# Kernel tuning notes

Hardware: AMD Instinct MI355X
Metric: run time of the kernel (lower is better)

## Reference

```python
import jax, jax.numpy as jnp
import numpy as np

EMBED = 768
GH = 4        # heads per group
GD = 256      # group dim = GH * head_dim
NSTEPS = 3    # n_pde_steps
DT = 0.05
HJ_H = 0.05   # Heimburg-Jackson dispersion coefficient


def _sh(u, k):
    # shift field content along sequence axis (axis=1) by k with zero boundary
    if k == 0:
        return u
    z = jnp.zeros_like(u)
    if k > 0:
        return z.at[:, k:, :].set(u[:, :-k, :])
    return z.at[:, :k, :].set(u[:, -k:, :])


def _d1(u):
    return 0.5 * (_sh(u, -1) - _sh(u, 1))


def _d2(u):
    return _sh(u, -1) - 2.0 * u + _sh(u, 1)


def _d3(u):
    return 0.5 * (_sh(u, -2) - 2.0 * _sh(u, -1) + 2.0 * _sh(u, 1) - _sh(u, 2))


def _d4(u):
    return _sh(u, -2) - 4.0 * _sh(u, -1) + 6.0 * u - 4.0 * _sh(u, 1) + _sh(u, 2)


def _attn(x, qkv_w, qkv_b, ow, ob, nh):
    # standard causal multi-head attention on one head group
    B, T, D = x.shape
    hd = D // nh
    qkv = x @ qkv_w + qkv_b                      # (B,T,3D)
    q, k, v = jnp.split(qkv, 3, axis=-1)
    heads = lambda a: a.reshape(B, T, nh, hd).transpose(0, 2, 1, 3)
    q, k, v = heads(q), heads(k), heads(v)
    s = jnp.einsum('bhqd,bhkd->bhqk', q, k) * (1.0 / np.sqrt(hd))
    causal = jnp.tril(jnp.ones((T, T), dtype=bool))
    s = jnp.where(causal, s, jnp.asarray(-1e9, s.dtype))
    p = jax.nn.softmax(s, axis=-1)
    o = jnp.einsum('bhqk,bhkd->bhqd', p, v).transpose(0, 2, 1, 3).reshape(B, T, D)
    return o @ ow + ob


def _sine_gordon(u):
    # u_tt = u_xx - sin(u), semi-implicit Euler (leapfrog-like)
    w = jnp.zeros_like(u)
    for _ in range(NSTEPS):
        w = w + DT * (_d2(u) - jnp.sin(u))
        u = u + DT * w
    return u


def _kdv(u):
    # u_t = -6 u u_x - u_xxx, explicit Euler
    for _ in range(NSTEPS):
        u = u + DT * (-6.0 * u * _d1(u) - _d3(u))
    return u


def _hj(u):
    # Heimburg-Jackson: u_tt = d_xx((c0^2 + p u + q u^2) u) - h u_xxxx
    # with c0=1, p=-1, q=1
    w = jnp.zeros_like(u)
    for _ in range(NSTEPS):
        f = u - u * u + u * u * u
        w = w + DT * (_d2(f) - HJ_H * _d4(u))
        u = u + DT * w
    return u


def setup_inputs() -> dict:
    key = jax.random.key(0)
    ks = jax.random.split(key, 16)
    s = 0.02
    d, gd = EMBED, GD
    inp = {'x': jax.random.normal(ks[0], (4, 2048, d), dtype=jnp.float32)}
    inp['in_w'] = jax.random.normal(ks[1], (d, d), jnp.float32) * s
    inp['in_b'] = jnp.zeros((d,), jnp.float32)
    for i, n in enumerate(['sg', 'kdv', 'hj']):
        inp[n + '_qkv_w'] = jax.random.normal(ks[2 + 4 * i], (gd, 3 * gd), jnp.float32) * s
        inp[n + '_qkv_b'] = jnp.zeros((3 * gd,), jnp.float32)
        inp[n + '_out_w'] = jax.random.normal(ks[3 + 4 * i], (gd, gd), jnp.float32) * s
        inp[n + '_out_b'] = jnp.zeros((gd,), jnp.float32)
    inp['out_w'] = jax.random.normal(ks[14], (d, d), jnp.float32) * s
    inp['out_b'] = jnp.zeros((d,), jnp.float32)
    return inp


def reference(x, in_w, in_b,
              sg_qkv_w, sg_qkv_b, sg_out_w, sg_out_b,
              kdv_qkv_w, kdv_qkv_b, kdv_out_w, kdv_out_b,
              hj_qkv_w, hj_qkv_b, hj_out_w, hj_out_b,
              out_w, out_b):
    h = x @ in_w + in_b
    xg = jnp.split(h, [GD, 2 * GD], axis=-1)
    sg = _sine_gordon(_attn(xg[0], sg_qkv_w, sg_qkv_b, sg_out_w, sg_out_b, GH))
    kv = _kdv(_attn(xg[1], kdv_qkv_w, kdv_qkv_b, kdv_out_w, kdv_out_b, GH))
    hj = _hj(_attn(xg[2], hj_qkv_w, hj_qkv_b, hj_out_w, hj_out_b, GH))
    out = jnp.concatenate([sg, kv, hj], axis=-1)
    return out @ out_w + out_b
```

## Files before the change

kernel.cpp:

```cpp
#include <hip/hip_runtime.h>
#include <math.h>

#define B_   4
#define T_   2048
#define D_   768
#define M_   8192
#define GD_  256
#define NH_  4
#define HD_  64

typedef short  s16x8 __attribute__((ext_vector_type(8)));
typedef __bf16 bfx8  __attribute__((ext_vector_type(8)));
typedef float  fx4   __attribute__((ext_vector_type(4)));

#define LOG2E 1.44269504088896f
#define QSCALE (0.125f * LOG2E)

__device__ __forceinline__ short f2bf(float f) {
  union { float f; unsigned u; } v; v.f = f;
  unsigned r = v.u + 0x7fffu + ((v.u >> 16) & 1u);
  return (short)(r >> 16);
}

__device__ __forceinline__ unsigned cvt_pk_bf16(float lo, float hi) {
  unsigned r;
  asm("v_cvt_pk_bf16_f32 %0, %1, %2" : "=v"(r) : "v"(lo), "v"(hi));
  return r;
}

__device__ __forceinline__ void gload16(const void* g, void* l) {
  __builtin_amdgcn_global_load_lds(
      (const __attribute__((address_space(1))) unsigned int*)g,
      (__attribute__((address_space(3))) unsigned int*)l, 16, 0, 0);
}

struct PW { const short* p0; const short* p1; const short* p2; };
struct PB { const float* p0; const float* p1; const float* p2; };
__device__ __forceinline__ const short* selw(const PW& s, int z) {
  return z == 0 ? s.p0 : (z == 1 ? s.p1 : s.p2);
}
__device__ __forceinline__ const float* selb(const PB& s, int z) {
  return z == 0 ? s.p0 : (z == 1 ? s.p1 : s.p2);
}

template<int AT, int OBF, int MODE, int BM>
__global__ __launch_bounds__(256) void gemm_mfma(
    const void* __restrict__ Avoid, long sA, int lda,
    PW Wp, PB Bp, int K,
    void* __restrict__ C, long sC, int ldc,
    void* __restrict__ xtra)
{
  constexpr int NF = BM / 32;
  constexpr int WTM = BM / 2;
  __shared__ short As[2][BM * 64];
  __shared__ short Bs[AT ? 1 : 2][128 * 64];

  const int z = blockIdx.z;
  const short* Ab16 = (const short*)Avoid + (long)z * sA;
  const float* Ab32 = (const float*)Avoid + (long)z * sA;
  const short* Wb = selw(Wp, z);
  const float* bb = selb(Bp, z);

  const int nx = gridDim.x, nwg = nx * gridDim.y;
  const int orig = blockIdx.y * nx + blockIdx.x;
  const int xcd = orig & 7, loc = orig >> 3;
  const int qq = nwg >> 3, rr = nwg & 7;
  const int wg = (xcd < rr ? xcd * (qq + 1) : rr * (qq + 1) + (xcd - rr) * qq) + loc;
  const int n0 = (wg % nx) * 128;
  const int m0 = (wg / nx) * BM;

  const int tid = threadIdx.x, lane = tid & 63, w = tid >> 6;
  const int wm = w >> 1, wn = w & 1;
  const int quad = lane >> 4, mr = lane & 15;

  fx4 acc[NF][4] = {};

  auto compute = [&](const short* Ab, const short* Bb) {
#pragma unroll
    for (int ks = 0; ks < 2; ++ks) {
      const int cc = ks * 32 + quad * 8;
      const int swz = cc ^ ((mr & 7) * 8);
      bfx8 af[NF], bf[4];
#pragma unroll
      for (int i = 0; i < NF; ++i)
        af[i] = *(const bfx8*)&Ab[(wm * WTM + i * 16 + mr) * 64 + swz];
#pragma unroll
      for (int j = 0; j < 4; ++j)
        bf[j] = *(const bfx8*)&Bb[(wn * 64 + j * 16 + mr) * 64 + swz];
#pragma unroll
      for (int i = 0; i < NF; ++i)
#pragma unroll
        for (int j = 0; j < 4; ++j)
          acc[i][j] = __builtin_amdgcn_mfma_f32_16x16x32_bf16(af[i], bf[j], acc[i][j], 0, 0, 0);
    }
  };

  if (AT) {
    const int r0 = tid >> 3;
    const int cs = (tid & 7) * 8;
    const int wswz = cs ^ ((r0 & 7) * 8);
    s16x8 ar[NF], br[4];

    auto loadA = [&](int k0) {
#pragma unroll
      for (int gg = 0; gg < NF; ++gg) {
        const float* p = Ab32 + (long)(m0 + r0 + 32 * gg) * lda + k0 + cs;
        float4 f0 = *(const float4*)p;
        float4 f1 = *(const float4*)(p + 4);
        short o[8] = { f2bf(f0.x), f2bf(f0.y), f2bf(f0.z), f2bf(f0.w),
                       f2bf(f1.x), f2bf(f1.y), f2bf(f1.z), f2bf(f1.w) };
        ar[gg] = *(s16x8*)o;
      }
    };
    auto loadB = [&](int k0) {
#pragma unroll
      for (int hh = 0; hh < 4; ++hh)
        br[hh] = *(const s16x8*)(Wb + (long)(n0 + r0 + 32 * hh) * K + k0 + cs);
    };

    loadA(0); loadB(0);
    for (int k0 = 0; k0 < K; k0 += 64) {
      asm volatile("s_waitcnt vmcnt(0)" ::: "memory");
#pragma unroll
      for (int gg = 0; gg < NF; ++gg)
        *(s16x8*)&As[0][(r0 + 32 * gg) * 64 + wswz] = ar[gg];
#pragma unroll
      for (int hh = 0; hh < 4; ++hh)
        *(s16x8*)&Bs[0][(r0 + 32 * hh) * 64 + wswz] = br[hh];
      asm volatile("s_waitcnt lgkmcnt(0)" ::: "memory");
      __builtin_amdgcn_s_barrier();
      if (k0 + 64 < K) { loadA(k0 + 64); loadB(k0 + 64); }
      compute(&As[0][0], &Bs[0][0]);
      __builtin_amdgcn_s_barrier();
    }
  } else {
    const int lrow = lane >> 3, lcol = lane & 7;

    auto stageA = [&](short* dst, int k0) {
#pragma unroll
      for (int i = 0; i < NF; ++i) {
        const int r = i * 32 + w * 8 + lrow;
        const int swz = (lcol * 8) ^ ((r & 7) * 8);
        gload16(Ab16 + (long)(m0 + r) * lda + k0 + swz,
                dst + (i * 32 + w * 8) * 64);
      }
    };
    auto stageB = [&](short* dst, int k0) {
#pragma unroll
      for (int i = 0; i < 4; ++i) {
        const int r = i * 32 + w * 8 + lrow;
        const int swz = (lcol * 8) ^ ((r & 7) * 8);
        gload16(Wb + (long)(n0 + r) * K + k0 + swz,
                dst + (i * 32 + w * 8) * 64);
      }
    };

    stageA(&As[0][0], 0); stageB(&Bs[0][0], 0);
    const int NT = K >> 6;
    for (int t = 0; t < NT; ++t) {
      const int cur = t & 1;
      if (t + 1 < NT) {
        stageA(&As[cur ^ 1][0], (t + 1) * 64);
        stageB(&Bs[cur ^ 1][0], (t + 1) * 64);
        if constexpr (BM == 128)
          asm volatile("s_waitcnt vmcnt(8)" ::: "memory");
        else
          asm volatile("s_waitcnt vmcnt(6)" ::: "memory");
      } else {
        asm volatile("s_waitcnt vmcnt(0)" ::: "memory");
      }
      __builtin_amdgcn_s_barrier();
      compute(&As[cur][0], &Bs[cur][0]);
      __builtin_amdgcn_s_barrier();
    }
  }

  float* Cf = (float*)C + (long)z * sC;
  short* Cs = (short*)C + (long)z * sC;
#pragma unroll
  for (int j = 0; j < 4; ++j) {
    const int col = n0 + wn * 64 + j * 16 + mr;
    const float bvx = bb[col];
#pragma unroll
    for (int i = 0; i < NF; ++i) {
      const int row0 = m0 + wm * WTM + i * 16 + quad * 4;
      if (MODE == 2) {
        const int rb = row0 >> 11, t0 = row0 & 2047;
        fx4 o;
#pragma unroll
        for (int r = 0; r < 4; ++r) o[r] = acc[i][j][r] + bvx;
        *(fx4*)((float*)xtra + (((long)z * B_ + rb) * GD_ + col) * T_ + t0) = o;
      } else if (MODE == 1 && col >= 512) {
        const int h = (col - 512) >> 6, hd = (col - 512) & 63;
        const int rb = row0 >> 11, t0 = row0 & 2047;
        short o4[4];
#pragma unroll
        for (int r = 0; r < 4; ++r) o4[r] = f2bf(acc[i][j][r] + bvx);
        *(short4*)((short*)xtra + ((((long)z * B_ + rb) * NH_ + h) * HD_ + hd) * T_ + t0) =
            *(short4*)o4;
      } else {
        const float sc = (MODE == 1 && col < 256) ? QSCALE : 1.0f;
#pragma unroll
        for (int r = 0; r < 4; ++r) {
          float v = (acc[i][j][r] + bvx) * sc;
          if (OBF) Cs[(long)(row0 + r) * ldc + col] = f2bf(v);
          else     Cf[(long)(row0 + r) * ldc + col] = v;
        }
      }
    }
  }
}

__global__ __launch_bounds__(256) void cvt_kernel(
    const float* __restrict__ x, short* __restrict__ xb)
{
  const size_t i = ((size_t)blockIdx.x * 256 + threadIdx.x) * 8;
  float4 f0 = *(const float4*)(x + i);
  float4 f1 = *(const float4*)(x + i + 4);
  short o[8] = { f2bf(f0.x), f2bf(f0.y), f2bf(f0.z), f2bf(f0.w),
                 f2bf(f1.x), f2bf(f1.y), f2bf(f1.z), f2bf(f1.w) };
  *(s16x8*)(xb + i) = *(s16x8*)o;
}

__global__ __launch_bounds__(256) void flash_attn_mfma(
    short* __restrict__ qkv, const short* __restrict__ vtb)
{
  __shared__ short Ks[64][72];
  __shared__ short Vs[80][72];
  __shared__ short Ps[64 * 64];

  const int bid = blockIdx.x;
  const int Q = 31 - (bid / 48);
  const int combo = bid % 48;
  const int g = combo % 3, bh = combo / 3;
  const int b = bh >> 2, h = bh & 3;

  short* base = qkv + ((size_t)g * M_ + (size_t)b * T_) * D_;
  short*       Qp = base + h * HD_;
  const short* Kp = base + GD_ + h * HD_;
  const short* Vtp = vtb + ((((size_t)g * B_ + b) * NH_ + h) * HD_) * T_;

  const int tid = threadIdx.x, lane = tid & 63, w = tid >> 6;
  const int quad = lane >> 4, mr = lane & 15;
  const int q0 = Q * 64, wr = w * 16;

  const int sra = tid >> 3, sc = (tid & 7) * 8;

  if (tid < 128) {
    const short ov = 0x3F80;
    s16x8 one = { ov, ov, ov, ov, ov, ov, ov, ov };
    *(s16x8*)&Vs[64 + (tid >> 3)][(tid & 7) * 8] = one;
  }

  bfx8 aq[2];
#pragma unroll
  for (int ks = 0; ks < 2; ++ks)
    aq[ks] = *(const bfx8*)(Qp + (size_t)(q0 + wr + mr) * D_ +
                            ks * 32 + quad * 8);

  s16x8 kreg0 = *(const s16x8*)(Kp + (size_t)sra * D_ + sc);
  s16x8 kreg1 = *(const s16x8*)(Kp + (size_t)(sra + 32) * D_ + sc);
  s16x8 vreg0 = *(const s16x8*)(Vtp + (size_t)sra * T_ + sc);
  s16x8 vreg1 = *(const s16x8*)(Vtp + (size_t)(sra + 32) * T_ + sc);

  fx4 Oa[5] = {};

  char* PsB = (char*)&Ps[0];
  const int rot = (mr & 7) << 4;

  for (int kt = 0; kt <= Q; ++kt) {
    *(s16x8*)&Ks[sra][sc]      = kreg0;
    *(s16x8*)&Ks[sra + 32][sc] = kreg1;
    *(s16x8*)&Vs[sra][sc]      = vreg0;
    *(s16x8*)&Vs[sra + 32][sc] = vreg1;
    __syncthreads();

    if (kt < Q) {
      const int kn = (kt + 1) * 64;
      kreg0 = *(const s16x8*)(Kp + (size_t)(kn + sra) * D_ + sc);
      kreg1 = *(const s16x8*)(Kp + (size_t)(kn + sra + 32) * D_ + sc);
      vreg0 = *(const s16x8*)(Vtp + (size_t)sra * T_ + kn + sc);
      vreg1 = *(const s16x8*)(Vtp + (size_t)(sra + 32) * T_ + kn + sc);
    }

    fx4 st[4] = {};
#pragma unroll
    for (int ks = 0; ks < 2; ++ks) {
      bfx8 bk[4];
#pragma unroll
      for (int jj = 0; jj < 4; ++jj)
        bk[jj] = *(const bfx8*)&Ks[jj * 16 + mr][ks * 32 + quad * 8];
#pragma unroll
      for (int jj = 0; jj < 4; ++jj)
        st[jj] = __builtin_amdgcn_mfma_f32_16x16x32_bf16(bk[jj], aq[ks], st[jj], 0, 0, 0);
    }

    if (kt == Q) {
      const int qg = q0 + wr + mr;
#pragma unroll
      for (int jj = 0; jj < 4; ++jj) {
        const int kvg0 = kt * 64 + jj * 16 + quad * 4;
#pragma unroll
        for (int r = 0; r < 4; ++r)
          if (kvg0 + r > qg) st[jj][r] = -1e30f;
      }
    }

    {
      const int rowb = (wr + mr) << 7;
#pragma unroll
      for (int jj = 0; jj < 4; ++jj) {
        float e0 = exp2f(st[jj][0]);
        float e1 = exp2f(st[jj][1]);
        float e2 = exp2f(st[jj][2]);
        float e3 = exp2f(st[jj][3]);
        unsigned pk0 = cvt_pk_bf16(e0, e1);
        unsigned pk1 = cvt_pk_bf16(e2, e3);
        unsigned long long pv = (unsigned long long)pk0 |
                                ((unsigned long long)pk1 << 32);
        const int kb = (jj * 32 + quad * 8) ^ rot;
        *(unsigned long long*)(PsB + rowb + kb) = pv;
      }
    }

#pragma unroll
    for (int ks = 0; ks < 2; ++ks) {
      const int rowb = (wr + mr) << 7;
      const int kb = (ks * 64 + quad * 16) ^ rot;
      bfx8 ap = *(const bfx8*)(PsB + rowb + kb);
#pragma unroll
      for (int j = 0; j < 5; ++j) {
        bfx8 bv = *(const bfx8*)&Vs[j * 16 + mr][ks * 32 + quad * 8];
        Oa[j] = __builtin_amdgcn_mfma_f32_16x16x32_bf16(ap, bv, Oa[j], 0, 0, 0);
      }
    }
    __syncthreads();
  }

#pragma unroll
  for (int r = 0; r < 4; ++r) {
    const float inv = 1.0f / Oa[4][r];
    const int row = q0 + wr + quad * 4 + r;
#pragma unroll
    for (int j = 0; j < 4; ++j)
      Qp[(size_t)row * D_ + j * 16 + mr] = f2bf(Oa[j][r] * inv);
  }
}

__device__ __forceinline__ float fhj(float x) { return x - x * x + x * x * x; }

__global__ __launch_bounds__(256) void pde_kernel(
    const float* __restrict__ ut, short* __restrict__ ubt)
{
  __shared__ float halo[3][2][4];

  const int cg = blockIdx.x, b = blockIdx.y, g = blockIdx.z;
  const int tid = threadIdx.x, w = tid >> 6, lane = tid & 63;
  const int c = w >> 1, half = w & 1;
  const int t0 = half * 1024 + lane * 16;
  const float dt = 0.05f;

  const float* src = ut + (((size_t)g * B_ + b) * GD_ + cg * 2 + c) * T_ + t0;

  float uc[20];
#pragma unroll
  for (int q = 0; q < 4; ++q)
    *(fx4*)&uc[2 + q * 4] = *(const fx4*)(src + q * 4);

  {
    float h0 = __shfl_up(uc[16], 1);
    float h1 = __shfl_up(uc[17], 1);
    float h2 = __shfl_down(uc[2], 1);
    float h3 = __shfl_down(uc[3], 1);
    if (half == 0 && lane == 63) { halo[0][c][0] = uc[16]; halo[0][c][1] = uc[17]; }
    if (half == 1 && lane == 0)  { halo[0][c][2] = uc[2];  halo[0][c][3] = uc[3]; }
    __syncthreads();
    uc[0] = h0; uc[1] = h1; uc[18] = h2; uc[19] = h3;
    if (lane == 0) {
      if (half == 1) { uc[0] = halo[0][c][0]; uc[1] = halo[0][c][1]; }
      else           { uc[0] = 0.f;           uc[1] = 0.f; }
    }
    if (lane == 63) {
      if (half == 0) { uc[18] = halo[0][c][2]; uc[19] = halo[0][c][3]; }
      else           { uc[18] = 0.f;           uc[19] = 0.f; }
    }
  }

  float wreg[16];
#pragma unroll
  for (int i = 0; i < 16; ++i) wreg[i] = 0.f;

  for (int step = 0; step < 3; ++step) {
    float nu[16];
#pragma unroll
    for (int tt = 0; tt < 16; ++tt) {
      float um2 = uc[tt], um1 = uc[tt + 1], u = uc[tt + 2];
      float up1 = uc[tt + 3], up2 = uc[tt + 4];
      if (g == 0) {
        float d2 = up1 - 2.f * u + um1;
        wreg[tt] += dt * (d2 - __sinf(u));
        nu[tt] = u + dt * wreg[tt];
      } else if (g == 1) {
        float d1 = 0.5f * (up1 - um1);
        float d3 = 0.5f * (up2 - 2.f * up1 + 2.f * um1 - um2);
        nu[tt] = u + dt * (-6.f * u * d1 - d3);
      } else {
        float d2f = fhj(up1) - 2.f * fhj(u) + fhj(um1);
        float d4  = up2 - 4.f * up1 + 6.f * u - 4.f * um1 + um2;
        wreg[tt] += dt * (d2f - 0.05f * d4);
        nu[tt] = u + dt * wreg[tt];
      }
    }
    if (step < 2) {
      float h0 = __shfl_up(nu[14], 1);
      float h1 = __shfl_up(nu[15], 1);
      float h2 = __shfl_down(nu[0], 1);
      float h3 = __shfl_down(nu[1], 1);
      if (half == 0 && lane == 63) { halo[step + 1][c][0] = nu[14]; halo[step + 1][c][1] = nu[15]; }
      if (half == 1 && lane == 0)  { halo[step + 1][c][2] = nu[0];  halo[step + 1][c][3] = nu[1]; }
      __syncthreads();
      uc[0] = h0; uc[1] = h1; uc[18] = h2; uc[19] = h3;
      if (lane == 0) {
        if (half == 1) { uc[0] = halo[step + 1][c][0]; uc[1] = halo[step + 1][c][1]; }
        else           { uc[0] = 0.f;                  uc[1] = 0.f; }
      }
      if (lane == 63) {
        if (half == 0) { uc[18] = halo[step + 1][c][2]; uc[19] = halo[step + 1][c][3]; }
        else           { uc[18] = 0.f;                  uc[19] = 0.f; }
      }
    }
#pragma unroll
    for (int i = 0; i < 16; ++i) uc[2 + i] = nu[i];
  }

  short o16[16];
#pragma unroll
  for (int i = 0; i < 16; ++i) o16[i] = f2bf(uc[2 + i]);
  short* dst = ubt + (((size_t)g * B_ + b) * GD_ + cg * 2 + c) * T_ + t0;
#pragma unroll
  for (int q = 0; q < 2; ++q)
    *(s16x8*)(dst + q * 8) = *(s16x8*)&o16[q * 8];
}

__global__ __launch_bounds__(256) void transp_kernel(
    const short* __restrict__ ubt, short* __restrict__ ub)
{
  __shared__ short Ls[32][264];

  const int tt = blockIdx.x;
  const int ct = blockIdx.y;
  const int z  = blockIdx.z;
  const int g = z >> 2, b = z & 3;
  const int tid = threadIdx.x;
  const int c0 = ct * 32, t0 = tt * 256;

  const short* src = ubt + (((size_t)g * B_ + b) * GD_ + c0) * T_ + t0;
#pragma unroll
  for (int it = 0; it < 4; ++it) {
    const int row = (tid >> 5) + it * 8;
    const int col = (tid & 31) * 8;
    *(s16x8*)&Ls[row][col] = *(const s16x8*)(src + (size_t)row * T_ + col);
  }
  __syncthreads();

  short* dst = ub + (size_t)b * T_ * D_ + g * GD_ + c0;
  const int cq = tid & 7, tr = tid >> 3;
#pragma unroll
  for (int p = 0; p < 8; ++p) {
    const int tl = p * 32 + tr;
    short o4[4];
#pragma unroll
    for (int i = 0; i < 4; ++i) o4[i] = Ls[cq * 4 + i][tl];
    *(short4*)(dst + (size_t)(t0 + tl) * D_ + cq * 4) = *(short4*)o4;
  }
}

struct PrepArgs {
  const float* w[8]; short* wt[8];
  int K[8], N[8];
  int tend[8];
};

__global__ __launch_bounds__(256) void prep_kernel(PrepArgs pa)
{
  const int bid = blockIdx.x, tid = threadIdx.x;
  __shared__ float Ws[32][33];
  int ti = 0;
#pragma unroll
  for (int i = 0; i < 8; ++i) if (bid >= pa.tend[i]) ti = i + 1;
  const int tloc = bid - (ti ? pa.tend[ti - 1] : 0);
  const int K = pa.K[ti], N = pa.N[ti];
  const int ntx = N >> 5;
  const int k0 = (tloc / ntx) * 32, n0 = (tloc % ntx) * 32;
  const float* W = pa.w[ti];
  short* WT = pa.wt[ti];
  const int tx = tid & 31, ty = tid >> 5;

#pragma unroll
  for (int i = 0; i < 4; ++i)
    Ws[ty + 8 * i][tx] = W[(long)(k0 + ty + 8 * i) * N + n0 + tx];
  __syncthreads();
#pragma unroll
  for (int i = 0; i < 4; ++i) {
    int r = ty + 8 * i;
    WT[(long)(n0 + r) * K + k0 + tx] = f2bf(Ws[tx][r]);
  }
}

extern "C" void kernel_launch(void* const* d_in, const int* in_sizes, int n_in,
                              void* d_out, int out_size, void* d_ws, size_t ws_size,
                              hipStream_t stream)
{
  (void)in_sizes; (void)n_in; (void)out_size; (void)ws_size;

  const float* x         = (const float*)d_in[0];
  const float* in_w      = (const float*)d_in[1];
  const float* in_b      = (const float*)d_in[2];
  const float* sg_qkv_w  = (const float*)d_in[3];
  const float* sg_qkv_b  = (const float*)d_in[4];
  const float* sg_out_w  = (const float*)d_in[5];
  const float* sg_out_b  = (const float*)d_in[6];
  const float* kdv_qkv_w = (const float*)d_in[7];
  const float* kdv_qkv_b = (const float*)d_in[8];
  const float* kdv_out_w = (const float*)d_in[9];
  const float* kdv_out_b = (const float*)d_in[10];
  const float* hj_qkv_w  = (const float*)d_in[11];
  const float* hj_qkv_b  = (const float*)d_in[12];
  const float* hj_out_w  = (const float*)d_in[13];
  const float* hj_out_b  = (const float*)d_in[14];
  const float* out_w     = (const float*)d_in[15];
  const float* out_b     = (const float*)d_in[16];
  float* out = (float*)d_out;

  const size_t MD = (size_t)M_ * D_;
  short* base = (short*)d_ws;
  short* xb   = base;
  short* hb   = base + MD;
  float* uf   = (float*)d_ws;
  short* qkvb = base + 2 * MD;
  short* ub16 = qkvb + 3 * MD;
  short* wts  = ub16 + MD;
  short* in_wT  = wts;
  short* qkvT0  = in_wT + 589824;
  short* qkvT1  = qkvT0 + 196608;
  short* qkvT2  = qkvT1 + 196608;
  short* outT0  = qkvT2 + 196608;
  short* outT1  = outT0 + 65536;
  short* outT2  = outT1 + 65536;
  short* out_wT = outT2 + 65536;
  short* vtb    = out_wT + 589824;
  short* ubt    = qkvb;

  dim3 blk(256);

  PrepArgs pa;
  const float* wsrc[8] = { in_w, sg_qkv_w, kdv_qkv_w, hj_qkv_w,
                           sg_out_w, kdv_out_w, hj_out_w, out_w };
  short* wdst[8] = { in_wT, qkvT0, qkvT1, qkvT2, outT0, outT1, outT2, out_wT };
  int Ksz[8] = { 768, 256, 256, 256, 256, 256, 256, 768 };
  int Nsz[8] = { 768, 768, 768, 768, 256, 256, 256, 768 };
  int cum = 0;
  for (int i = 0; i < 8; ++i) {
    pa.w[i] = wsrc[i]; pa.wt[i] = wdst[i]; pa.K[i] = Ksz[i]; pa.N[i] = Nsz[i];
    cum += (Ksz[i] >> 5) * (Nsz[i] >> 5);
    pa.tend[i] = cum;
  }
  prep_kernel<<<dim3((unsigned)cum), blk, 0, stream>>>(pa);
  cvt_kernel<<<dim3((unsigned)(MD / 2048)), blk, 0, stream>>>(x, xb);

  gemm_mfma<0, 1, 0, 64><<<dim3(6, 128, 1), blk, 0, stream>>>(
      xb, 0, D_, PW{in_wT, in_wT, in_wT}, PB{in_b, in_b, in_b}, D_,
      hb, 0, D_, nullptr);

  gemm_mfma<0, 1, 1, 64><<<dim3(6, 128, 3), blk, 0, stream>>>(
      hb, 256, D_,
      PW{qkvT0, qkvT1, qkvT2}, PB{sg_qkv_b, kdv_qkv_b, hj_qkv_b}, GD_,
      qkvb, (long)MD, D_, vtb);

  flash_attn_mfma<<<dim3(1536), blk, 0, stream>>>(qkvb, vtb);

  gemm_mfma<0, 0, 2, 64><<<dim3(2, 128, 3), blk, 0, stream>>>(
      qkvb, (long)MD, D_,
      PW{outT0, outT1, outT2}, PB{sg_out_b, kdv_out_b, hj_out_b}, GD_,
      uf, 0, 0, uf);

  pde_kernel<<<dim3(128, 4, 3), blk, 0, stream>>>(uf, ubt);

  transp_kernel<<<dim3(8, 8, 12), blk, 0, stream>>>(ubt, ub16);

  gemm_mfma<0, 0, 0, 64><<<dim3(6, 128, 1), blk, 0, stream>>>(
      ub16, 0, D_, PW{out_wT, out_wT, out_wT}, PB{out_b, out_b, out_b}, D_,
      out, 0, D_, nullptr);
}
```

Baseline: 257.6 us.

## Double flash-attention query tile to 128 rows with 512-thread blocks

Each attention block now covers 128 query rows using 8 waves instead of 64 rows with 4 waves, so every K/V tile staged in shared memory is reused by twice as many waves. Each thread loads one K and one V vector per tile instead of two, and the grid is halved. Waves whose rows lie entirely before the current causal tile skip the compute but still join the barriers, which adds some idle time on the diagonal tiles and lowers the number of blocks available to fill the GPU.

```diff
diff --git a/kernel.cpp b/kernel.cpp
--- a/kernel.cpp
+++ b/kernel.cpp
@@ -222,15 +222,15 @@
   *(s16x8*)(xb + i) = *(s16x8*)o;
 }
 
-__global__ __launch_bounds__(256) void flash_attn_mfma(
+__global__ __launch_bounds__(512) void flash_attn_mfma(
     short* __restrict__ qkv, const short* __restrict__ vtb)
 {
   __shared__ short Ks[64][72];
   __shared__ short Vs[80][72];
-  __shared__ short Ps[64 * 64];
+  __shared__ short Ps[128 * 64];
 
   const int bid = blockIdx.x;
-  const int Q = 31 - (bid / 48);
+  const int Q = 15 - (bid / 48);
   const int combo = bid % 48;
   const int g = combo % 3, bh = combo / 3;
   const int b = bh >> 2, h = bh & 3;
@@ -242,7 +242,8 @@
 
   const int tid = threadIdx.x, lane = tid & 63, w = tid >> 6;
   const int quad = lane >> 4, mr = lane & 15;
-  const int q0 = Q * 64, wr = w * 16;
+  const int q0 = Q * 128, wr = w * 16;
+  const int qhi = q0 + wr + 15;
 
   const int sra = tid >> 3, sc = (tid & 7) * 8;
 
@@ -258,80 +259,77 @@
     aq[ks] = *(const bfx8*)(Qp + (size_t)(q0 + wr + mr) * D_ +
                             ks * 32 + quad * 8);
 
-  s16x8 kreg0 = *(const s16x8*)(Kp + (size_t)sra * D_ + sc);
-  s16x8 kreg1 = *(const s16x8*)(Kp + (size_t)(sra + 32) * D_ + sc);
-  s16x8 vreg0 = *(const s16x8*)(Vtp + (size_t)sra * T_ + sc);
-  s16x8 vreg1 = *(const s16x8*)(Vtp + (size_t)(sra + 32) * T_ + sc);
+  s16x8 kreg = *(const s16x8*)(Kp + (size_t)sra * D_ + sc);
+  s16x8 vreg = *(const s16x8*)(Vtp + (size_t)sra * T_ + sc);
 
   fx4 Oa[5] = {};
 
   char* PsB = (char*)&Ps[0];
   const int rot = (mr & 7) << 4;
 
-  for (int kt = 0; kt <= Q; ++kt) {
-    *(s16x8*)&Ks[sra][sc]      = kreg0;
-    *(s16x8*)&Ks[sra + 32][sc] = kreg1;
-    *(s16x8*)&Vs[sra][sc]      = vreg0;
-    *(s16x8*)&Vs[sra + 32][sc] = vreg1;
+  const int ktmax = 2 * Q + 1;
+  for (int kt = 0; kt <= ktmax; ++kt) {
+    *(s16x8*)&Ks[sra][sc] = kreg;
+    *(s16x8*)&Vs[sra][sc] = vreg;
     __syncthreads();
 
-    if (kt < Q) {
+    if (kt < ktmax) {
       const int kn = (kt + 1) * 64;
-      kreg0 = *(const s16x8*)(Kp + (size_t)(kn + sra) * D_ + sc);
-      kreg1 = *(const s16x8*)(Kp + (size_t)(kn + sra + 32) * D_ + sc);
-      vreg0 = *(const s16x8*)(Vtp + (size_t)sra * T_ + kn + sc);
-      vreg1 = *(const s16x8*)(Vtp + (size_t)(sra + 32) * T_ + kn + sc);
-    }
-
-    fx4 st[4] = {};
-#pragma unroll
-    for (int ks = 0; ks < 2; ++ks) {
-      bfx8 bk[4];
-#pragma unroll
-      for (int jj = 0; jj < 4; ++jj)
-        bk[jj] = *(const bfx8*)&Ks[jj * 16 + mr][ks * 32 + quad * 8];
-#pragma unroll
-      for (int jj = 0; jj < 4; ++jj)
-        st[jj] = __builtin_amdgcn_mfma_f32_16x16x32_bf16(bk[jj], aq[ks], st[jj], 0, 0, 0);
-    }
-
-    if (kt == Q) {
-      const int qg = q0 + wr + mr;
-#pragma unroll
-      for (int jj = 0; jj < 4; ++jj) {
-        const int kvg0 = kt * 64 + jj * 16 + quad * 4;
-#pragma unroll
-        for (int r = 0; r < 4; ++r)
-          if (kvg0 + r > qg) st[jj][r] = -1e30f;
-      }
-    }
-
-    {
-      const int rowb = (wr + mr) << 7;
-#pragma unroll
-      for (int jj = 0; jj < 4; ++jj) {
-        float e0 = exp2f(st[jj][0]);
-        float e1 = exp2f(st[jj][1]);
-        float e2 = exp2f(st[jj][2]);
-        float e3 = exp2f(st[jj][3]);
-        unsigned pk0 = cvt_pk_bf16(e0, e1);
-        unsigned pk1 = cvt_pk_bf16(e2, e3);
-        unsigned long long pv = (unsigned long long)pk0 |
-                                ((unsigned long long)pk1 << 32);
-        const int kb = (jj * 32 + quad * 8) ^ rot;
-        *(unsigned long long*)(PsB + rowb + kb) = pv;
-      }
-    }
-
-#pragma unroll
-    for (int ks = 0; ks < 2; ++ks) {
-      const int rowb = (wr + mr) << 7;
-      const int kb = (ks * 64 + quad * 16) ^ rot;
-      bfx8 ap = *(const bfx8*)(PsB + rowb + kb);
-#pragma unroll
-      for (int j = 0; j < 5; ++j) {
-        bfx8 bv = *(const bfx8*)&Vs[j * 16 + mr][ks * 32 + quad * 8];
-        Oa[j] = __builtin_amdgcn_mfma_f32_16x16x32_bf16(ap, bv, Oa[j], 0, 0, 0);
+      kreg = *(const s16x8*)(Kp + (size_t)(kn + sra) * D_ + sc);
+      vreg = *(const s16x8*)(Vtp + (size_t)sra * T_ + kn + sc);
+    }
+
+    if (kt * 64 <= qhi) {
+      fx4 st[4] = {};
+#pragma unroll
+      for (int ks = 0; ks < 2; ++ks) {
+        bfx8 bk[4];
+#pragma unroll
+        for (int jj = 0; jj < 4; ++jj)
+          bk[jj] = *(const bfx8*)&Ks[jj * 16 + mr][ks * 32 + quad * 8];
+#pragma unroll
+        for (int jj = 0; jj < 4; ++jj)
+          st[jj] = __builtin_amdgcn_mfma_f32_16x16x32_bf16(bk[jj], aq[ks], st[jj], 0, 0, 0);
+      }
+
+      if (kt >= 2 * Q) {
+        const int qg = q0 + wr + mr;
+#pragma unroll
+        for (int jj = 0; jj < 4; ++jj) {
+          const int kvg0 = kt * 64 + jj * 16 + quad * 4;
+#pragma unroll
+          for (int r = 0; r < 4; ++r)
+            if (kvg0 + r > qg) st[jj][r] = -1e30f;
+        }
+      }
+
+      {
+        const int rowb = (wr + mr) << 7;
+#pragma unroll
+        for (int jj = 0; jj < 4; ++jj) {
+          float e0 = exp2f(st[jj][0]);
+          float e1 = exp2f(st[jj][1]);
+          float e2 = exp2f(st[jj][2]);
+          float e3 = exp2f(st[jj][3]);
+          unsigned pk0 = cvt_pk_bf16(e0, e1);
+          unsigned pk1 = cvt_pk_bf16(e2, e3);
+          unsigned long long pv = (unsigned long long)pk0 |
+                                  ((unsigned long long)pk1 << 32);
+          const int kb = (jj * 32 + quad * 8) ^ rot;
+          *(unsigned long long*)(PsB + rowb + kb) = pv;
+        }
+      }
+
+#pragma unroll
+      for (int ks = 0; ks < 2; ++ks) {
+        const int rowb = (wr + mr) << 7;
+        const int kb = (ks * 64 + quad * 16) ^ rot;
+        bfx8 ap = *(const bfx8*)(PsB + rowb + kb);
+#pragma unroll
+        for (int j = 0; j < 5; ++j) {
+          bfx8 bv = *(const bfx8*)&Vs[j * 16 + mr][ks * 32 + quad * 8];
+          Oa[j] = __builtin_amdgcn_mfma_f32_16x16x32_bf16(ap, bv, Oa[j], 0, 0, 0);
+        }
       }
     }
     __syncthreads();
@@ -577,7 +575,7 @@
       PW{qkvT0, qkvT1, qkvT2}, PB{sg_qkv_b, kdv_qkv_b, hj_qkv_b}, GD_,
       qkvb, (long)MD, D_, vtb);
 
-  flash_attn_mfma<<<dim3(1536), blk, 0, stream>>>(qkvb, vtb);
+  flash_attn_mfma<<<dim3(768), dim3(512), 0, stream>>>(qkvb, vtb);
 
   gemm_mfma<0, 0, 2, 64><<<dim3(2, 128, 3), blk, 0, stream>>>(
       qkvb, (long)MD, D_,
```

After: 252.3 us. 1.02x faster.
